# Performance work log

Hardware: AMD Instinct MI355X
Metric: run time of the kernel (lower is better)

Reference implementation:

```python
import jax, jax.numpy as jnp
import numpy as np

DIM = 32          # image/vq dim (ImageTransform3D default dim=32 == vq.layers[0].dim)
CODEBOOK = 1024   # number of codebook entries
TOTAL = 4194304   # flat weight-vector length (multiple of DIM)


def setup_inputs() -> dict:
    key = jax.random.key(0)
    k1, k2, k3 = jax.random.split(key, 3)
    weights = jax.random.normal(k1, (TOTAL,), dtype=jnp.float32)
    condition = jax.random.normal(k2, (1, DIM, TOTAL // DIM), dtype=jnp.float32)
    codebook = jax.random.normal(k3, (CODEBOOK, DIM), dtype=jnp.float32)
    return {"weights": weights, "condition": condition, "codebook": codebook}


def reference(weights, condition, codebook):
    # --- ImageTransform3D.forward: pad flat weights to a multiple of DIM, view (1, DIM, -1)
    pad = (-weights.shape[0]) % DIM  # static
    if pad:
        weights = jnp.concatenate([weights, jnp.zeros((pad,), weights.dtype)])
    img = weights.reshape(1, DIM, -1)
    # --- TokenTransform3D: subtract condition, flatten to tokens of size DIM
    x = (img - condition).reshape(-1, DIM)  # [N, DIM]
    # --- VectorQuantize (freeze_codebook, eval): nearest-neighbour lookup
    d = (
        jnp.sum(x * x, axis=-1, keepdims=True)
        - 2.0 * (x @ codebook.T)
        + jnp.sum(codebook * codebook, axis=-1)
    )
    indices = jnp.argmin(d, axis=-1)  # [N] int32
    return indices
```

## Files before the change

kernel.cpp:

```cpp
#include <hip/hip_runtime.h>

#define TOTAL     4194304
#define DIM       32
#define NTOK      (TOTAL / DIM)
#define NCODE     1024
#define CCODES    256
#define DELTA_EPS 2e-3f
#define FLAGBIT   0x40000000

typedef _Float16 half8   __attribute__((ext_vector_type(8)));
typedef float    floatx4 __attribute__((ext_vector_type(4)));

#define GLOAD_LDS16(g, l) \
    __builtin_amdgcn_global_load_lds((const __attribute__((address_space(1))) void*)(g), \
                                     (__attribute__((address_space(3))) void*)(l), 16, 0, 0)
#define GLOAD_LDS4(g, l) \
    __builtin_amdgcn_global_load_lds((const __attribute__((address_space(1))) void*)(g), \
                                     (__attribute__((address_space(3))) void*)(l), 4, 0, 0)

__global__ __launch_bounds__(64) void vq_prep(
    const float* __restrict__ cb, float* __restrict__ nhb,
    _Float16* __restrict__ Eh, _Float16* __restrict__ El,
    float* __restrict__ cbT)
{
    const int k = blockIdx.x * 64 + threadIdx.x;
    const float4* e4 = reinterpret_cast<const float4*>(cb) + (size_t)k * 8;
    float v[DIM];
    float4 t[8];
#pragma unroll
    for (int j = 0; j < 8; ++j) t[j] = e4[j];
#pragma unroll
    for (int j = 0; j < 8; ++j) {
        v[4 * j + 0] = t[j].x; v[4 * j + 1] = t[j].y;
        v[4 * j + 2] = t[j].z; v[4 * j + 3] = t[j].w;
    }
    float e2 = 0.0f;
#pragma unroll
    for (int i = 0; i < DIM; ++i) e2 = fmaf(v[i], v[i], e2);
    nhb[k] = -0.5f * e2;

#pragma unroll
    for (int j = 0; j < DIM; ++j) cbT[(size_t)j * NCODE + k] = v[j];

    const int chunk = k >> 8, within = k & 255;
    const int step = within >> 4, l15 = within & 15;
#pragma unroll
    for (int l4 = 0; l4 < 4; ++l4) {
        half8 h, lo;
#pragma unroll
        for (int j = 0; j < 8; ++j) {
            float x = v[l4 * 8 + j];
            _Float16 hh = (_Float16)x;
            h[j]  = hh;
            lo[j] = (_Float16)(x - (float)hh);
        }
        const int slot = chunk * 1024 + step * 64 + l4 * 16 + l15;
        *reinterpret_cast<half8*>(Eh + (size_t)slot * 8) = h;
        *reinterpret_cast<half8*>(El + (size_t)slot * 8) = lo;
    }
}

__global__ __launch_bounds__(256) void vq_main(
    const float* __restrict__ w, const float* __restrict__ c,
    const float* __restrict__ nhb, const _Float16* __restrict__ Eh,
    const _Float16* __restrict__ El, const float* __restrict__ cbT,
    int* __restrict__ out)
{
    __shared__ _Float16 sEh[1024 * 8];
    __shared__ _Float16 sEl[1024 * 8];
    __shared__ float    snh[CCODES];
    __shared__ int      sOut[128];
    __shared__ float    sXf[4][DIM];

    const int tid  = threadIdx.x;
    const int lane = tid & 63;
    const int wid  = tid >> 6;
    const int tokw = blockIdx.x * 128 + wid * 32;
    const int l15  = lane & 15;
    const int l4   = lane >> 4;

    half8 xh[2], xl[2];
#pragma unroll
    for (int m = 0; m < 2; ++m) {
        const int token = tokw + m * 16 + l15;
        const float4* pw = reinterpret_cast<const float4*>(w + (size_t)token * DIM + l4 * 8);
        const float4* pc = reinterpret_cast<const float4*>(c + (size_t)token * DIM + l4 * 8);
        float4 a0 = pw[0], a1 = pw[1], b0 = pc[0], b1 = pc[1];
        float xs[8] = {a0.x - b0.x, a0.y - b0.y, a0.z - b0.z, a0.w - b0.w,
                       a1.x - b1.x, a1.y - b1.y, a1.z - b1.z, a1.w - b1.w};
#pragma unroll
        for (int j = 0; j < 8; ++j) {
            _Float16 h = (_Float16)xs[j];
            xh[m][j] = h;
            xl[m][j] = (_Float16)(xs[j] - (float)h);
        }
    }

    const float NEGINF = __uint_as_float(0xFF800000u);
    float best[8], second[8];
#pragma unroll
    for (int q = 0; q < 8; ++q) { best[q] = NEGINF; second[q] = NEGINF; }

    for (int ch = 0; ch < 4; ++ch) {
        if (ch) __syncthreads();
        {
            const _Float16* gh = Eh + (size_t)ch * 8192;
            const _Float16* gl = El + (size_t)ch * 8192;
#pragma unroll
            for (int r2 = 0; r2 < 4; ++r2) {
                const int slot = r2 * 256 + wid * 64;
                GLOAD_LDS16(gh + (size_t)(slot + lane) * 8, sEh + (size_t)slot * 8);
                GLOAD_LDS16(gl + (size_t)(slot + lane) * 8, sEl + (size_t)slot * 8);
            }
            GLOAD_LDS4(nhb + ch * CCODES + wid * 64 + lane, snh + wid * 64);
        }
        __syncthreads();

#pragma unroll
        for (int sp = 0; sp < 8; ++sp) {
            const int sA = 2 * sp, sB = 2 * sp + 1;
            const half8 ehA = *reinterpret_cast<const half8*>(sEh + (size_t)(sA * 64 + lane) * 8);
            const half8 elA = *reinterpret_cast<const half8*>(sEl + (size_t)(sA * 64 + lane) * 8);
            const half8 ehB = *reinterpret_cast<const half8*>(sEh + (size_t)(sB * 64 + lane) * 8);
            const half8 elB = *reinterpret_cast<const half8*>(sEl + (size_t)(sB * 64 + lane) * 8);
            const float nhA = snh[sA * 16 + l15];
            const float nhB = snh[sB * 16 + l15];
            const unsigned ixA = 1023u - (unsigned)(ch * CCODES + sA * 16 + l15);
            const unsigned ixB = ixA - 16u;
            const floatx4 nA = {nhA, nhA, nhA, nhA};
            const floatx4 nB = {nhB, nhB, nhB, nhB};
#pragma unroll
            for (int m = 0; m < 2; ++m) {
                floatx4 aA = __builtin_amdgcn_mfma_f32_16x16x32_f16(xh[m], ehA, nA, 0, 0, 0);
                aA = __builtin_amdgcn_mfma_f32_16x16x32_f16(xl[m], ehA, aA, 0, 0, 0);
                aA = __builtin_amdgcn_mfma_f32_16x16x32_f16(xh[m], elA, aA, 0, 0, 0);
                floatx4 aB = __builtin_amdgcn_mfma_f32_16x16x32_f16(xh[m], ehB, nB, 0, 0, 0);
                aB = __builtin_amdgcn_mfma_f32_16x16x32_f16(xl[m], ehB, aB, 0, 0, 0);
                aB = __builtin_amdgcn_mfma_f32_16x16x32_f16(xh[m], elB, aB, 0, 0, 0);
#pragma unroll
                for (int r = 0; r < 4; ++r) {
                    const int q = m * 4 + r;
                    float pA = __uint_as_float((__float_as_uint(aA[r]) & 0xFFFFFC00u) | ixA);
                    float pB = __uint_as_float((__float_as_uint(aB[r]) & 0xFFFFFC00u) | ixB);
                    second[q] = fmaxf(second[q], __builtin_amdgcn_fmed3f(pA, pB, best[q]));
                    best[q]   = fmaxf(fmaxf(best[q], pA), pB);
                }
            }
        }
    }

#pragma unroll
    for (int sh = 1; sh < 16; sh <<= 1) {
#pragma unroll
        for (int q = 0; q < 8; ++q) {
            float bB = __shfl_xor(best[q], sh);
            float sB = __shfl_xor(second[q], sh);
            second[q] = fmaxf(fmaxf(second[q], sB), fminf(best[q], bB));
            best[q]   = fmaxf(best[q], bB);
        }
    }

    if (l15 == 0) {
#pragma unroll
        for (int m = 0; m < 2; ++m) {
#pragma unroll
            for (int r = 0; r < 4; ++r) {
                const int q = m * 4 + r;
                unsigned ub = __float_as_uint(best[q]);
                unsigned us = __float_as_uint(second[q]);
                float bv = __uint_as_float(ub & 0xFFFFFC00u);
                float sv = __uint_as_float(us & 0xFFFFFC00u);
                int eb = (int)((ub >> 23) & 255u);
                int es = (int)((us >> 23) & 255u);
                int em = eb > es ? eb : es;
                em = em > 12 ? em : 12;
                float thr = __uint_as_float((unsigned)(em - 11) << 23) + DELTA_EPS;
                int k = 1023 - (int)(ub & 1023u);
                sOut[wid * 32 + m * 16 + l4 * 4 + r] = ((bv - sv) < thr) ? (k | FLAGBIT) : k;
            }
        }
    }

    int myval = 0;
    if (lane < 32) myval = sOut[wid * 32 + lane];
    unsigned long long mask = __ballot(lane < 32 && (myval & FLAGBIT));
    while (mask) {
        const int src = __ffsll(mask) - 1;
        mask &= mask - 1;
        const int token = tokw + src;

        if (lane < DIM)
            sXf[wid][lane] = w[(size_t)token * DIM + lane] - c[(size_t)token * DIM + lane];

        float x2 = 0.f;
#pragma unroll
        for (int i = 0; i < DIM; ++i) x2 = fmaf(sXf[wid][i], sXf[wid][i], x2);

        float dmin = INFINITY;
        int   kbest = 0;
        for (int i = 0; i < 16; ++i) {
            const int k = lane + 64 * i;
            float dot = 0.f;
#pragma unroll
            for (int j = 0; j < DIM; ++j)
                dot = fmaf(sXf[wid][j], cbT[(size_t)j * NCODE + k], dot);
            float e2 = -2.0f * nhb[k];
            float dd = fmaf(-2.0f, dot, x2) + e2;
            if (dd < dmin) { dmin = dd; kbest = k; }
        }
#pragma unroll
        for (int sh = 1; sh < 64; sh <<= 1) {
            float dB = __shfl_xor(dmin, sh);
            int   iB = __shfl_xor(kbest, sh);
            bool take = (dB < dmin) || (dB == dmin && iB < kbest);
            dmin = take ? dB : dmin;
            kbest = take ? iB : kbest;
        }
        if (lane == src) myval = kbest;
    }
    if (lane < 32) out[tokw + lane] = myval;
}

extern "C" void kernel_launch(void* const* d_in, const int* in_sizes, int n_in,
                              void* d_out, int out_size, void* d_ws, size_t ws_size,
                              hipStream_t stream) {
    const float* w  = (const float*)d_in[0];
    const float* c  = (const float*)d_in[1];
    const float* cb = (const float*)d_in[2];
    int* out = (int*)d_out;

    char* wsb = (char*)d_ws;
    float*    nhb = (float*)wsb;
    _Float16* Eh  = (_Float16*)(wsb + 4096);
    _Float16* El  = (_Float16*)(wsb + 4096 + 65536);
    float*    cbT = (float*)(wsb + 4096 + 65536 + 65536);

    vq_prep<<<NCODE / 64, 64, 0, stream>>>(cb, nhb, Eh, El, cbT);
    vq_main<<<NTOK / 128, 256, 0, stream>>>(w, c, nhb, Eh, El, cbT, out);
}
```

Measured before the change: 55.88 us.

## Split codebook across two blocks per token tile and merge in separate kernel

The main kernel now processes half of the codebook per block, doubling the grid to 2048 blocks and halving LDS use so more blocks fit per CU. Each block writes per-token best/second scores to workspace, and a new merge kernel combines the halves, applies the ambiguity threshold and runs the exact fp32 fallback for flagged tokens. The split is meant to raise occupancy and parallelism, at the cost of a third kernel launch, extra global traffic for the partial results, and re-reading x inside the fallback. The threshold exponent offset also changes from 11 to 12.

Measured after the change: 71.22 us. 1.27x slower.

```diff
diff --git a/kernel.cpp b/kernel.cpp
--- a/kernel.cpp
+++ b/kernel.cpp
@@ -4,7 +4,7 @@
 #define DIM       32
 #define NTOK      (TOTAL / DIM)
 #define NCODE     1024
-#define CCODES    256
+#define CCODES    128
 #define DELTA_EPS 2e-3f
 #define FLAGBIT   0x40000000
 
@@ -42,7 +42,7 @@
 #pragma unroll
     for (int j = 0; j < DIM; ++j) cbT[(size_t)j * NCODE + k] = v[j];
 
-    const int chunk = k >> 8, within = k & 255;
+    const int chunk = k >> 7, within = k & 127;
     const int step = within >> 4, l15 = within & 15;
 #pragma unroll
     for (int l4 = 0; l4 < 4; ++l4) {
@@ -54,7 +54,7 @@
             h[j]  = hh;
             lo[j] = (_Float16)(x - (float)hh);
         }
-        const int slot = chunk * 1024 + step * 64 + l4 * 16 + l15;
+        const int slot = chunk * 512 + step * 64 + l4 * 16 + l15;
         *reinterpret_cast<half8*>(Eh + (size_t)slot * 8) = h;
         *reinterpret_cast<half8*>(El + (size_t)slot * 8) = lo;
     }
@@ -63,19 +63,18 @@
 __global__ __launch_bounds__(256) void vq_main(
     const float* __restrict__ w, const float* __restrict__ c,
     const float* __restrict__ nhb, const _Float16* __restrict__ Eh,
-    const _Float16* __restrict__ El, const float* __restrict__ cbT,
-    int* __restrict__ out)
+    const _Float16* __restrict__ El, float2* __restrict__ wsBS)
 {
-    __shared__ _Float16 sEh[1024 * 8];
-    __shared__ _Float16 sEl[1024 * 8];
+    __shared__ _Float16 sEh[512 * 8];
+    __shared__ _Float16 sEl[512 * 8];
     __shared__ float    snh[CCODES];
-    __shared__ int      sOut[128];
-    __shared__ float    sXf[4][DIM];
 
     const int tid  = threadIdx.x;
     const int lane = tid & 63;
     const int wid  = tid >> 6;
-    const int tokw = blockIdx.x * 128 + wid * 32;
+    const int half = blockIdx.x & 1;
+    const int tok0 = (blockIdx.x >> 1) * 128;
+    const int tokw = tok0 + wid * 32;
     const int l15  = lane & 15;
     const int l4   = lane >> 4;
 
@@ -101,23 +100,24 @@
 #pragma unroll
     for (int q = 0; q < 8; ++q) { best[q] = NEGINF; second[q] = NEGINF; }
 
-    for (int ch = 0; ch < 4; ++ch) {
-        if (ch) __syncthreads();
+    for (int cc = 0; cc < 4; ++cc) {
+        const int ch = half * 4 + cc;
+        if (cc) __syncthreads();
         {
-            const _Float16* gh = Eh + (size_t)ch * 8192;
-            const _Float16* gl = El + (size_t)ch * 8192;
-#pragma unroll
-            for (int r2 = 0; r2 < 4; ++r2) {
+            const _Float16* gh = Eh + (size_t)ch * 4096;
+            const _Float16* gl = El + (size_t)ch * 4096;
+#pragma unroll
+            for (int r2 = 0; r2 < 2; ++r2) {
                 const int slot = r2 * 256 + wid * 64;
                 GLOAD_LDS16(gh + (size_t)(slot + lane) * 8, sEh + (size_t)slot * 8);
                 GLOAD_LDS16(gl + (size_t)(slot + lane) * 8, sEl + (size_t)slot * 8);
             }
-            GLOAD_LDS4(nhb + ch * CCODES + wid * 64 + lane, snh + wid * 64);
+            if (wid < 2) GLOAD_LDS4(nhb + ch * CCODES + wid * 64 + lane, snh + wid * 64);
         }
         __syncthreads();
 
 #pragma unroll
-        for (int sp = 0; sp < 8; ++sp) {
+        for (int sp = 0; sp < 4; ++sp) {
             const int sA = 2 * sp, sB = 2 * sp + 1;
             const half8 ehA = *reinterpret_cast<const half8*>(sEh + (size_t)(sA * 64 + lane) * 8);
             const half8 elA = *reinterpret_cast<const half8*>(sEl + (size_t)(sA * 64 + lane) * 8);
@@ -166,28 +166,50 @@
 #pragma unroll
             for (int r = 0; r < 4; ++r) {
                 const int q = m * 4 + r;
-                unsigned ub = __float_as_uint(best[q]);
-                unsigned us = __float_as_uint(second[q]);
-                float bv = __uint_as_float(ub & 0xFFFFFC00u);
-                float sv = __uint_as_float(us & 0xFFFFFC00u);
-                int eb = (int)((ub >> 23) & 255u);
-                int es = (int)((us >> 23) & 255u);
-                int em = eb > es ? eb : es;
-                em = em > 12 ? em : 12;
-                float thr = __uint_as_float((unsigned)(em - 11) << 23) + DELTA_EPS;
-                int k = 1023 - (int)(ub & 1023u);
-                sOut[wid * 32 + m * 16 + l4 * 4 + r] = ((bv - sv) < thr) ? (k | FLAGBIT) : k;
+                const int token = tokw + m * 16 + l4 * 4 + r;
+                wsBS[(size_t)half * NTOK + token] = make_float2(best[q], second[q]);
             }
         }
     }
-
-    int myval = 0;
-    if (lane < 32) myval = sOut[wid * 32 + lane];
-    unsigned long long mask = __ballot(lane < 32 && (myval & FLAGBIT));
+}
+
+__global__ __launch_bounds__(256) void vq_merge(
+    const float* __restrict__ w, const float* __restrict__ c,
+    const float* __restrict__ cbT, const float* __restrict__ nhb,
+    const float2* __restrict__ wsBS, int* __restrict__ out)
+{
+    __shared__ float sXf[4][DIM];
+
+    const int tid  = threadIdx.x;
+    const int lane = tid & 63;
+    const int wid  = tid >> 6;
+    const int t    = blockIdx.x * 256 + tid;
+    const int tbase = blockIdx.x * 256 + wid * 64;
+
+    float2 a = wsBS[t];
+    float2 b = wsBS[(size_t)NTOK + t];
+    float best   = fmaxf(a.x, b.x);
+    float second = fmaxf(fmaxf(a.y, b.y), fminf(a.x, b.x));
+
+    unsigned ub = __float_as_uint(best);
+    unsigned us = __float_as_uint(second);
+    float bv = __uint_as_float(ub & 0xFFFFFC00u);
+    float sv = __uint_as_float(us & 0xFFFFFC00u);
+    int eb = (int)((ub >> 23) & 255u);
+    int es = (int)((us >> 23) & 255u);
+    int em = eb > es ? eb : es;
+    em = em > 12 ? em : 12;
+    float thr = __uint_as_float((unsigned)(em - 12) << 23) + DELTA_EPS;
+    int k = 1023 - (int)(ub & 1023u);
+    int myval = ((bv - sv) < thr) ? (k | FLAGBIT) : k;
+
+    unsigned long long mask = __ballot((myval & FLAGBIT) != 0);
+    if (!(myval & FLAGBIT)) out[t] = myval;
+
     while (mask) {
         const int src = __ffsll(mask) - 1;
         mask &= mask - 1;
-        const int token = tokw + src;
+        const int token = tbase + src;
 
         if (lane < DIM)
             sXf[wid][lane] = w[(size_t)token * DIM + lane] - c[(size_t)token * DIM + lane];
@@ -199,14 +221,14 @@
         float dmin = INFINITY;
         int   kbest = 0;
         for (int i = 0; i < 16; ++i) {
-            const int k = lane + 64 * i;
+            const int kk = lane + 64 * i;
             float dot = 0.f;
 #pragma unroll
-            for (int j = 0; j < DIM; ++j)
-                dot = fmaf(sXf[wid][j], cbT[(size_t)j * NCODE + k], dot);
-            float e2 = -2.0f * nhb[k];
+            for (int jj = 0; jj < DIM; ++jj)
+                dot = fmaf(sXf[wid][jj], cbT[(size_t)jj * NCODE + kk], dot);
+            float e2 = -2.0f * nhb[kk];
             float dd = fmaf(-2.0f, dot, x2) + e2;
-            if (dd < dmin) { dmin = dd; kbest = k; }
+            if (dd < dmin) { dmin = dd; kbest = kk; }
         }
 #pragma unroll
         for (int sh = 1; sh < 64; sh <<= 1) {
@@ -216,9 +238,8 @@
             dmin = take ? dB : dmin;
             kbest = take ? iB : kbest;
         }
-        if (lane == src) myval = kbest;
-    }
-    if (lane < 32) out[tokw + lane] = myval;
+        if (lane == 0) out[token] = kbest;
+    }
 }
 
 extern "C" void kernel_launch(void* const* d_in, const int* in_sizes, int n_in,
@@ -230,11 +251,13 @@
     int* out = (int*)d_out;
 
     char* wsb = (char*)d_ws;
-    float*    nhb = (float*)wsb;
-    _Float16* Eh  = (_Float16*)(wsb + 4096);
-    _Float16* El  = (_Float16*)(wsb + 4096 + 65536);
-    float*    cbT = (float*)(wsb + 4096 + 65536 + 65536);
+    float*    nhb  = (float*)wsb;
+    _Float16* Eh   = (_Float16*)(wsb + 4096);
+    _Float16* El   = (_Float16*)(wsb + 4096 + 65536);
+    float*    cbT  = (float*)(wsb + 4096 + 2 * 65536);
+    float2*   wsBS = (float2*)(wsb + 4096 + 2 * 65536 + 131072);
 
     vq_prep<<<NCODE / 64, 64, 0, stream>>>(cb, nhb, Eh, El, cbT);
-    vq_main<<<NTOK / 128, 256, 0, stream>>>(w, c, nhb, Eh, El, cbT, out);
-}
+    vq_main<<<2 * (NTOK / 128), 256, 0, stream>>>(w, c, nhb, Eh, El, wsBS);
+    vq_merge<<<NTOK / 256, 256, 0, stream>>>(w, c, cbT, nhb, wsBS, out);
+}
```
